# Kernel optimization log

Hardware: AMD Instinct MI355X
Metric: run time of the kernel (lower is better)

The kernel has to match this reference:

```python
import jax, jax.numpy as jnp
import numpy as np

THRESH = 0.5  # global `thresh` used by ActFun (NOT init_thresh)
LENS = 0.5    # global `lens` (surrogate window)
DECAY = 0.25  # init_decay


@jax.custom_vjp
def act_fun(u):
    return (u > THRESH).astype(u.dtype)

def _act_fwd(u):
    return act_fun(u), u

def _act_bwd(u, g):
    surrogate = (jnp.abs(u - THRESH) < LENS).astype(g.dtype) / (2.0 * LENS)
    return (g * surrogate,)

act_fun.defvjp(_act_fwd, _act_bwd)


def setup_inputs() -> dict:
    key = jax.random.key(0)
    x = jax.random.normal(key, (32, 256, 4096), dtype=jnp.float32)  # [T, B, D]
    return {"x": x}


def reference(x):
    # LIF recurrence: mem_t = mem_{t-1} * decay * (1 - stop_grad(spike_{t-1})) + x_t
    mem0 = x[0]
    spike0 = act_fun(mem0)

    def step(carry, x_t):
        mem, spike = carry
        mem = mem * DECAY * (1.0 - jax.lax.stop_gradient(spike)) + x_t
        s = act_fun(mem)
        return (mem, s), s

    _, spikes = jax.lax.scan(step, (mem0, spike0), x[1:])
    return jnp.concatenate([spike0[None], spikes], axis=0)  # [T, B, D]
```

## Files before the change

kernel.cpp:

```cpp
#include <hip/hip_runtime.h>


constexpr int   T_STEPS = 32;
constexpr float THRESH  = 0.5f;
constexpr float DECAY   = 0.25f;

__global__ __launch_bounds__(256) void lif_fwd_kernel(
    const float4* __restrict__ x,
    float4* __restrict__ out,
    int n4)
{
    int i = blockIdx.x * 256 + threadIdx.x;
    if (i >= n4) return;

    float4 mem = x[i];
    float4 s;
    s.x = mem.x > THRESH ? 1.0f : 0.0f;
    s.y = mem.y > THRESH ? 1.0f : 0.0f;
    s.z = mem.z > THRESH ? 1.0f : 0.0f;
    s.w = mem.w > THRESH ? 1.0f : 0.0f;
    out[i] = s;

#pragma unroll
    for (int t = 1; t < T_STEPS; ++t) {
        float4 xv = x[t * n4 + i];
        mem.x = mem.x * (DECAY * (1.0f - s.x)) + xv.x;
        mem.y = mem.y * (DECAY * (1.0f - s.y)) + xv.y;
        mem.z = mem.z * (DECAY * (1.0f - s.z)) + xv.z;
        mem.w = mem.w * (DECAY * (1.0f - s.w)) + xv.w;
        s.x = mem.x > THRESH ? 1.0f : 0.0f;
        s.y = mem.y > THRESH ? 1.0f : 0.0f;
        s.z = mem.z > THRESH ? 1.0f : 0.0f;
        s.w = mem.w > THRESH ? 1.0f : 0.0f;
        out[t * n4 + i] = s;
    }
}

extern "C" void kernel_launch(void* const* d_in, const int* in_sizes, int n_in,
                              void* d_out, int out_size, void* d_ws, size_t ws_size,
                              hipStream_t stream) {
    const float* x = (const float*)d_in[0];
    float* out = (float*)d_out;

    const int total = in_sizes[0];
    const int n     = total / T_STEPS;
    const int n4    = n / 4;

    const int block = 256;
    const int grid  = (n4 + block - 1) / block;

    lif_fwd_kernel<<<grid, block, 0, stream>>>(
        reinterpret_cast<const float4*>(x),
        reinterpret_cast<float4*>(out),
        n4);
}
```

Measured before the change: 232.0 us.

## Double-buffer timestep loads in register chunks and use nontemporal stores

Loads the input in chunks of eight timesteps into two register buffers, so the next chunk's loads are issued while the current chunk is computed. This keeps many more memory requests in flight per thread. Spike outputs are written with nontemporal stores so the write stream does not pollute the cache. The cost is higher register pressure (up to 64 float4 values live), which may lower occupancy.

```diff
diff --git a/kernel.cpp b/kernel.cpp
--- a/kernel.cpp
+++ b/kernel.cpp
@@ -2,8 +2,41 @@
 
 
 constexpr int   T_STEPS = 32;
+constexpr int   CHUNK   = 8;
 constexpr float THRESH  = 0.5f;
 constexpr float DECAY   = 0.25f;
+
+typedef float v4f __attribute__((ext_vector_type(4)));
+
+__device__ __forceinline__ void load_chunk(float4* buf, const float4* __restrict__ xp,
+                                           int t0, int n4) {
+#pragma unroll
+    for (int k = 0; k < CHUNK; ++k)
+        buf[k] = xp[(t0 + k) * n4];
+}
+
+template <int T0>
+__device__ __forceinline__ void compute_chunk(const float4* buf, float4& mem, float4& s,
+                                              float4* __restrict__ op, int n4) {
+#pragma unroll
+    for (int k = 0; k < CHUNK; ++k) {
+        float4 v = buf[k];
+        if (T0 + k == 0) {
+            mem = v;
+        } else {
+            mem.x = mem.x * (DECAY * (1.0f - s.x)) + v.x;
+            mem.y = mem.y * (DECAY * (1.0f - s.y)) + v.y;
+            mem.z = mem.z * (DECAY * (1.0f - s.z)) + v.z;
+            mem.w = mem.w * (DECAY * (1.0f - s.w)) + v.w;
+        }
+        s.x = mem.x > THRESH ? 1.0f : 0.0f;
+        s.y = mem.y > THRESH ? 1.0f : 0.0f;
+        s.z = mem.z > THRESH ? 1.0f : 0.0f;
+        s.w = mem.w > THRESH ? 1.0f : 0.0f;
+        v4f sv = {s.x, s.y, s.z, s.w};
+        __builtin_nontemporal_store(sv, (v4f*)(op + (T0 + k) * n4));
+    }
+}
 
 __global__ __launch_bounds__(256) void lif_fwd_kernel(
     const float4* __restrict__ x,
@@ -13,27 +46,20 @@
     int i = blockIdx.x * 256 + threadIdx.x;
     if (i >= n4) return;
 
-    float4 mem = x[i];
-    float4 s;
-    s.x = mem.x > THRESH ? 1.0f : 0.0f;
-    s.y = mem.y > THRESH ? 1.0f : 0.0f;
-    s.z = mem.z > THRESH ? 1.0f : 0.0f;
-    s.w = mem.w > THRESH ? 1.0f : 0.0f;
-    out[i] = s;
+    const float4* xp = x + i;
+    float4*       op = out + i;
 
-#pragma unroll
-    for (int t = 1; t < T_STEPS; ++t) {
-        float4 xv = x[t * n4 + i];
-        mem.x = mem.x * (DECAY * (1.0f - s.x)) + xv.x;
-        mem.y = mem.y * (DECAY * (1.0f - s.y)) + xv.y;
-        mem.z = mem.z * (DECAY * (1.0f - s.z)) + xv.z;
-        mem.w = mem.w * (DECAY * (1.0f - s.w)) + xv.w;
-        s.x = mem.x > THRESH ? 1.0f : 0.0f;
-        s.y = mem.y > THRESH ? 1.0f : 0.0f;
-        s.z = mem.z > THRESH ? 1.0f : 0.0f;
-        s.w = mem.w > THRESH ? 1.0f : 0.0f;
-        out[t * n4 + i] = s;
-    }
+    float4 bufA[CHUNK], bufB[CHUNK];
+    float4 mem, s;
+
+    load_chunk(bufA, xp, 0, n4);
+    load_chunk(bufB, xp, 8, n4);
+    compute_chunk<0>(bufA, mem, s, op, n4);
+    load_chunk(bufA, xp, 16, n4);
+    compute_chunk<8>(bufB, mem, s, op, n4);
+    load_chunk(bufB, xp, 24, n4);
+    compute_chunk<16>(bufA, mem, s, op, n4);
+    compute_chunk<24>(bufB, mem, s, op, n4);
 }
 
 extern "C" void kernel_launch(void* const* d_in, const int* in_sizes, int n_in,
```

Result: no change. 230.9 us (-0.5%).

## Use float2 lanes with double-buffered register prefetch of time steps

Applied to the files above, without the earlier changes.

Each thread now handles two elements through float2 accesses instead of four through float4, which doubles the thread count. Inputs for the time steps are prefetched eight ahead in two register buffers, and the time loop is left rolled at the outer level. The launch bounds now request eight blocks per CU, aiming to keep more memory requests in flight across the 32 serial steps. The step-zero case is handled by starting mem and spike at zero, which gives the same result because the first step's decay term multiplies zero. The risks are narrower memory transactions and redundant clamped loads at the tail.

```diff
diff --git a/kernel.cpp b/kernel.cpp
--- a/kernel.cpp
+++ b/kernel.cpp
@@ -2,37 +2,61 @@
 
 
 constexpr int   T_STEPS = 32;
+constexpr int   CHUNK   = 4;
 constexpr float THRESH  = 0.5f;
 constexpr float DECAY   = 0.25f;
 
-__global__ __launch_bounds__(256) void lif_fwd_kernel(
-    const float4* __restrict__ x,
-    float4* __restrict__ out,
-    int n4)
-{
-    int i = blockIdx.x * 256 + threadIdx.x;
-    if (i >= n4) return;
-
-    float4 mem = x[i];
-    float4 s;
+__device__ __forceinline__ void lif_step(float2& mem, float2& s, float2 v) {
+    mem.x = mem.x * (DECAY * (1.0f - s.x)) + v.x;
+    mem.y = mem.y * (DECAY * (1.0f - s.y)) + v.y;
     s.x = mem.x > THRESH ? 1.0f : 0.0f;
     s.y = mem.y > THRESH ? 1.0f : 0.0f;
-    s.z = mem.z > THRESH ? 1.0f : 0.0f;
-    s.w = mem.w > THRESH ? 1.0f : 0.0f;
-    out[i] = s;
+}
+
+__global__ __launch_bounds__(256, 8) void lif_fwd_kernel(
+    const float2* __restrict__ x,
+    float2* __restrict__ out,
+    int n2)
+{
+    const int i = blockIdx.x * 256 + threadIdx.x;
+    if (i >= n2) return;
+
+    const float2* xp = x + i;
+    float2*       op = out + i;
+
+    float2 A[CHUNK], B[CHUNK];
 
 #pragma unroll
-    for (int t = 1; t < T_STEPS; ++t) {
-        float4 xv = x[t * n4 + i];
-        mem.x = mem.x * (DECAY * (1.0f - s.x)) + xv.x;
-        mem.y = mem.y * (DECAY * (1.0f - s.y)) + xv.y;
-        mem.z = mem.z * (DECAY * (1.0f - s.z)) + xv.z;
-        mem.w = mem.w * (DECAY * (1.0f - s.w)) + xv.w;
-        s.x = mem.x > THRESH ? 1.0f : 0.0f;
-        s.y = mem.y > THRESH ? 1.0f : 0.0f;
-        s.z = mem.z > THRESH ? 1.0f : 0.0f;
-        s.w = mem.w > THRESH ? 1.0f : 0.0f;
-        out[t * n4 + i] = s;
+    for (int k = 0; k < CHUNK; ++k) A[k] = xp[k * n2];
+#pragma unroll
+    for (int k = 0; k < CHUNK; ++k) B[k] = xp[(CHUNK + k) * n2];
+
+    float2 mem = {0.0f, 0.0f};
+    float2 s   = {0.0f, 0.0f};
+
+#pragma unroll 1
+    for (int cc = 0; cc < T_STEPS / (2 * CHUNK); ++cc) {
+        const int t0 = cc * 2 * CHUNK;
+
+#pragma unroll
+        for (int k = 0; k < CHUNK; ++k) {
+            float2 v = A[k];
+            int tp = t0 + 2 * CHUNK + k;
+            tp = tp < T_STEPS - 1 ? tp : T_STEPS - 1;
+            A[k] = xp[tp * n2];
+            lif_step(mem, s, v);
+            op[(t0 + k) * n2] = s;
+        }
+
+#pragma unroll
+        for (int k = 0; k < CHUNK; ++k) {
+            float2 v = B[k];
+            int tp = t0 + 3 * CHUNK + k;
+            tp = tp < T_STEPS - 1 ? tp : T_STEPS - 1;
+            B[k] = xp[tp * n2];
+            lif_step(mem, s, v);
+            op[(t0 + CHUNK + k) * n2] = s;
+        }
     }
 }
 
@@ -44,13 +68,13 @@
 
     const int total = in_sizes[0];
     const int n     = total / T_STEPS;
-    const int n4    = n / 4;
+    const int n2    = n / 2;
 
     const int block = 256;
-    const int grid  = (n4 + block - 1) / block;
+    const int grid  = (n2 + block - 1) / block;
 
     lif_fwd_kernel<<<grid, block, 0, stream>>>(
-        reinterpret_cast<const float4*>(x),
-        reinterpret_cast<float4*>(out),
-        n4);
+        reinterpret_cast<const float2*>(x),
+        reinterpret_cast<float2*>(out),
+        n2);
 }
```

After: 235.2 us. Within noise of the previous version (+1.4%).

## Split LIF time recurrence into four chunked kernels with workspace carry

Applied to the files above, without the earlier changes.

Splits the 32-step scan into four kernel launches of 8 steps each, passing the membrane state through a workspace buffer between launches. The spike state is recomputed from the carried membrane, and the first chunk starts from zero state, which gives the same result as the original. The apparent aim is to change the memory access pattern or scheduling across time chunks. The cost is extra carry reads and writes plus three more launches on a kernel that is purely memory bound.

```diff
diff --git a/kernel.cpp b/kernel.cpp
--- a/kernel.cpp
+++ b/kernel.cpp
@@ -1,56 +1,65 @@
 #include <hip/hip_runtime.h>
 
 
-constexpr int   T_STEPS = 32;
-constexpr float THRESH  = 0.5f;
-constexpr float DECAY   = 0.25f;
+constexpr float THRESH = 0.5f;
+constexpr float DECAY  = 0.25f;
 
-__global__ __launch_bounds__(256) void lif_fwd_kernel(
+template <int T0, int TN, bool WRITE_CARRY>
+__global__ __launch_bounds__(256) void lif_chunk_kernel(
     const float4* __restrict__ x,
     float4* __restrict__ out,
+    float4* __restrict__ carry,
     int n4)
 {
-    int i = blockIdx.x * 256 + threadIdx.x;
+    const int i = blockIdx.x * 256 + threadIdx.x;
     if (i >= n4) return;
 
-    float4 mem = x[i];
-    float4 s;
-    s.x = mem.x > THRESH ? 1.0f : 0.0f;
-    s.y = mem.y > THRESH ? 1.0f : 0.0f;
-    s.z = mem.z > THRESH ? 1.0f : 0.0f;
-    s.w = mem.w > THRESH ? 1.0f : 0.0f;
-    out[i] = s;
-
-#pragma unroll
-    for (int t = 1; t < T_STEPS; ++t) {
-        float4 xv = x[t * n4 + i];
-        mem.x = mem.x * (DECAY * (1.0f - s.x)) + xv.x;
-        mem.y = mem.y * (DECAY * (1.0f - s.y)) + xv.y;
-        mem.z = mem.z * (DECAY * (1.0f - s.z)) + xv.z;
-        mem.w = mem.w * (DECAY * (1.0f - s.w)) + xv.w;
+    float4 mem, s;
+    if (T0 == 0) {
+        mem = {0.0f, 0.0f, 0.0f, 0.0f};
+        s   = {0.0f, 0.0f, 0.0f, 0.0f};
+    } else {
+        mem = carry[i];
         s.x = mem.x > THRESH ? 1.0f : 0.0f;
         s.y = mem.y > THRESH ? 1.0f : 0.0f;
         s.z = mem.z > THRESH ? 1.0f : 0.0f;
         s.w = mem.w > THRESH ? 1.0f : 0.0f;
-        out[t * n4 + i] = s;
     }
+
+#pragma unroll
+    for (int t = 0; t < TN; ++t) {
+        float4 v = x[(T0 + t) * n4 + i];
+        mem.x = mem.x * (DECAY * (1.0f - s.x)) + v.x;
+        mem.y = mem.y * (DECAY * (1.0f - s.y)) + v.y;
+        mem.z = mem.z * (DECAY * (1.0f - s.z)) + v.z;
+        mem.w = mem.w * (DECAY * (1.0f - s.w)) + v.w;
+        s.x = mem.x > THRESH ? 1.0f : 0.0f;
+        s.y = mem.y > THRESH ? 1.0f : 0.0f;
+        s.z = mem.z > THRESH ? 1.0f : 0.0f;
+        s.w = mem.w > THRESH ? 1.0f : 0.0f;
+        out[(T0 + t) * n4 + i] = s;
+    }
+
+    if (WRITE_CARRY)
+        carry[i] = mem;
 }
 
 extern "C" void kernel_launch(void* const* d_in, const int* in_sizes, int n_in,
                               void* d_out, int out_size, void* d_ws, size_t ws_size,
                               hipStream_t stream) {
-    const float* x = (const float*)d_in[0];
-    float* out = (float*)d_out;
+    const float4* x     = reinterpret_cast<const float4*>(d_in[0]);
+    float4*       out   = reinterpret_cast<float4*>(d_out);
+    float4*       carry = reinterpret_cast<float4*>(d_ws);
 
     const int total = in_sizes[0];
-    const int n     = total / T_STEPS;
+    const int n     = total / 32;
     const int n4    = n / 4;
 
     const int block = 256;
     const int grid  = (n4 + block - 1) / block;
 
-    lif_fwd_kernel<<<grid, block, 0, stream>>>(
-        reinterpret_cast<const float4*>(x),
-        reinterpret_cast<float4*>(out),
-        n4);
+    lif_chunk_kernel< 0, 8, true ><<<grid, block, 0, stream>>>(x, out, carry, n4);
+    lif_chunk_kernel< 8, 8, true ><<<grid, block, 0, stream>>>(x, out, carry, n4);
+    lif_chunk_kernel<16, 8, true ><<<grid, block, 0, stream>>>(x, out, carry, n4);
+    lif_chunk_kernel<24, 8, false><<<grid, block, 0, stream>>>(x, out, carry, n4);
 }
```

After: 236.8 us. 2.1% more time.
